# Kernel tuning notes

Measured on AMD Instinct MI355X. Metric: run time of the kernel, lower is better.

The kernel has to match this reference:

```python
import jax, jax.numpy as jnp
import numpy as np

N = 10000      # nodes
E = 65536      # edges
IN = 16        # in_channels
H = 64         # hidden_channels
ED = 4         # edge_attr_dim
MLP_H = 64     # hidden width of edge-weight MLPs


def _glorot(key, shape):
    fan_in, fan_out = shape[0], shape[1]
    lim = np.sqrt(6.0 / (fan_in + fan_out)).astype(np.float32)
    return jax.random.uniform(key, shape, jnp.float32, -lim, lim)


def setup_inputs() -> dict:
    key = jax.random.key(0)
    ks = jax.random.split(key, 16)
    x = jax.random.normal(ks[0], (N, IN), dtype=jnp.float32)
    edge_index = jax.random.randint(ks[1], (2, E), 0, N, dtype=jnp.int64)
    edge_attr = jax.random.normal(ks[2], (E, ED), dtype=jnp.float32)
    return {
        "x": x,
        "edge_index": edge_index,
        "edge_attr": edge_attr,
        # nn1: Linear(ED,64) -> ReLU -> Linear(64, IN*H)
        "nn1_w1": _glorot(ks[3], (ED, MLP_H)), "nn1_b1": jnp.zeros((MLP_H,), jnp.float32),
        "nn1_w2": _glorot(ks[4], (MLP_H, IN * H)), "nn1_b2": jnp.zeros((IN * H,), jnp.float32),
        "root1": _glorot(ks[5], (IN, H)), "bias1": jnp.zeros((H,), jnp.float32),
        # nn2: Linear(ED,64) -> ReLU -> Linear(64, H*H)
        "nn2_w1": _glorot(ks[6], (ED, MLP_H)), "nn2_b1": jnp.zeros((MLP_H,), jnp.float32),
        "nn2_w2": _glorot(ks[7], (MLP_H, H * H)), "nn2_b2": jnp.zeros((H * H,), jnp.float32),
        "root2": _glorot(ks[8], (H, H)), "bias2": jnp.zeros((H,), jnp.float32),
        # readout MLP
        "lin1_w": _glorot(ks[9], (H, 8)), "lin1_b": jnp.zeros((8,), jnp.float32),
        "lin2_w": _glorot(ks[10], (8, 1)), "lin2_b": jnp.zeros((1,), jnp.float32),
    }


def _nnconv(x, src, dst, edge_attr, w1, b1, w2, b2, root, bias, cin, cout):
    # Edge-conditioned weight generation: MLP(edge_attr) -> [E, cin, cout]
    h = jax.nn.relu(edge_attr @ w1 + b1)
    We = (h @ w2 + b2).reshape(-1, cin, cout)
    # Per-edge matmul: message_e = x[src_e] @ We_e  -> [E, cout]
    msg = jnp.einsum('ei,eio->eo', x[src], We)
    # Scatter mean over destination nodes
    s = jax.ops.segment_sum(msg, dst, num_segments=N)
    cnt = jax.ops.segment_sum(jnp.ones((msg.shape[0],), x.dtype), dst, num_segments=N)
    agg = s / jnp.maximum(cnt, 1.0)[:, None]
    # Root transform + bias (PyG NNConv defaults: root_weight=True, bias=True)
    return agg + x @ root + bias


def reference(x, edge_index, edge_attr,
              nn1_w1, nn1_b1, nn1_w2, nn1_b2, root1, bias1,
              nn2_w1, nn2_b1, nn2_w2, nn2_b2, root2, bias2,
              lin1_w, lin1_b, lin2_w, lin2_b):
    # Dropout layers are identity in eval mode.
    src, dst = edge_index[0], edge_index[1]
    h = jax.nn.relu(_nnconv(x, src, dst, edge_attr,
                            nn1_w1, nn1_b1, nn1_w2, nn1_b2, root1, bias1, IN, H))
    h = jax.nn.relu(_nnconv(h, src, dst, edge_attr,
                            nn2_w1, nn2_b1, nn2_w2, nn2_b2, root2, bias2, H, H))
    h = jax.nn.relu(h @ lin1_w + lin1_b)
    return (h @ lin2_w + lin2_b)[:, 0]  # squeeze(-1) -> [N]
```

## Files before the change

kernel.cpp:

```cpp
#include <hip/hip_runtime.h>
#include <hip/hip_bf16.h>

#define NN 10000
#define EE 65536

using short8  = __attribute__((ext_vector_type(8))) short;
using u16x8   = __attribute__((ext_vector_type(8))) unsigned short;
using float4v = __attribute__((ext_vector_type(4))) float;

__device__ __forceinline__ unsigned short f2b(float f){
  union { float f; unsigned int u; } v; v.f = f;
  unsigned int u = v.u;
  unsigned int r = (u + 0x7fff + ((u >> 16) & 1)) >> 16;
  return (unsigned short)r;
}



__device__ __forceinline__ void do_permB(int idx, const float* __restrict__ w2,
                                         unsigned short* __restrict__ Bt,
                                         int cin, int s , int cb ){
  int tile   = idx >> 9;
  int within = idx & 511;
  int ot  = tile >> s;
  int k32 = tile & ((1<<s)-1);
  int kklo = within & 7;
  int q    = within >> 3;
  int kkhi = q & 3;
  int orow = q >> 2;
  int o = ot*16 + orow;
  int k = k32*32 + kkhi*8 + kklo;
  int m = k >> cb;
  int i = k & (cin-1);
  Bt[idx] = f2b(w2[(size_t)m*(cin*64) + i*64 + o]);
}

__global__ __launch_bounds__(256) void k_prep(
    const float* __restrict__ w2a, unsigned short* __restrict__ Bt1,
    const float* __restrict__ w2b, unsigned short* __restrict__ Bt2,
    int* __restrict__ cnt){
  int b = blockIdx.x;
  int t = threadIdx.x;
  if(b < 40){
    int i = b*256 + t;
    if(i < NN) cnt[i] = 0;
  } else if(b < 296){
    do_permB((b-40)*256 + t, w2a, Bt1, 16, 5, 4);
  } else {
    do_permB((b-296)*256 + t, w2b, Bt2, 64, 7, 6);
  }
}


__global__ void k_hist(const int* __restrict__ dst, int* __restrict__ cnt){
  int e = blockIdx.x*256 + threadIdx.x;
  if(e < EE) atomicAdd(&cnt[dst[e]], 1);
}

__global__ __launch_bounds__(1024) void k_scan(const int* __restrict__ cnt, int* __restrict__ offs, int* __restrict__ cursor){
  const int T = 1024, PER = (NN + T - 1)/T;
  int tid = threadIdx.x;
  int base = tid*PER;
  int local[PER];
  int s = 0;
  #pragma unroll
  for(int j=0;j<PER;j++){
    int i = base+j;
    int v = (i<NN)? cnt[i] : 0;
    local[j] = s;
    s += v;
  }
  int lane = tid & 63, wv = tid >> 6;
  int val = s;
  #pragma unroll
  for(int o=1;o<64;o<<=1){
    int u = __shfl_up(val, o, 64);
    if(lane >= o) val += u;
  }
  __shared__ int wsum[16];
  if(lane==63) wsum[wv] = val;
  __syncthreads();
  if(tid==0){
    int acc=0;
    #pragma unroll
    for(int i=0;i<16;i++){ int t2=wsum[i]; wsum[i]=acc; acc+=t2; }
  }
  __syncthreads();
  int thr_excl = wsum[wv] + (val - s);
  #pragma unroll
  for(int j=0;j<PER;j++){
    int i = base+j;
    if(i<NN){ int e = thr_excl + local[j]; offs[i]=e; cursor[i]=e; }
  }
  if(tid == T-1) offs[NN] = thr_excl + s;
}

__global__ void k_scatter(const int* __restrict__ dst, const int* __restrict__ src,
                          int* __restrict__ cursor, int2* __restrict__ elist2){
  int e = blockIdx.x*256 + threadIdx.x;
  if(e < EE){ int p = atomicAdd(&cursor[dst[e]], 1); elist2[p] = make_int2(e, src[e]); }
}


__global__ __launch_bounds__(64) void k_accK1(const float* __restrict__ x,
    const int* __restrict__ offs, const int2* __restrict__ elist2,
    const float* __restrict__ ea, const float* __restrict__ w1, const float* __restrict__ b1,
    unsigned short* __restrict__ K1, float* __restrict__ XS, int v0){
  int v = v0 + blockIdx.x;
  int L = threadIdx.x;
  int cg = L & 3, mg = L >> 2;
  int i0 = cg << 2;
  float w1c0 = w1[L], w1c1 = w1[64+L], w1c2 = w1[128+L], w1c3 = w1[192+L];
  float b1c = b1[L];
  __shared__ float sh[2][64];
  float acc[4][4];
  #pragma unroll
  for(int j=0;j<4;j++)
    #pragma unroll
    for(int c=0;c<4;c++) acc[j][c]=0.f;
  float4 xs = make_float4(0.f,0.f,0.f,0.f);
  int p0 = offs[v], p1 = offs[v+1];
  float4 a_nxt = make_float4(0.f,0.f,0.f,0.f);
  float4 x_nxt = make_float4(0.f,0.f,0.f,0.f);
  if(p0 < p1){
    int2 es = elist2[p0];
    a_nxt = *(const float4*)(ea + (size_t)es.x*4);
    x_nxt = *(const float4*)(x + (size_t)es.y*16 + i0);
  }
  for(int p=p0;p<p1;p++){
    int buf = (p-p0)&1;
    float4 xv = x_nxt;
    float4 av = a_nxt;
    float hv = fmaxf(b1c + av.x*w1c0 + av.y*w1c1 + av.z*w1c2 + av.w*w1c3, 0.f);
    sh[buf][L] = hv;
    __syncthreads();
    if(p+1<p1){
      int2 es = elist2[p+1];
      a_nxt = *(const float4*)(ea + (size_t)es.x*4);
      x_nxt = *(const float4*)(x + (size_t)es.y*16 + i0);
    }
    xs.x += xv.x; xs.y += xv.y; xs.z += xv.z; xs.w += xv.w;
    #pragma unroll
    for(int j=0;j<4;j++){
      float hm = sh[buf][mg + 16*j];
      acc[j][0] += hm*xv.x; acc[j][1] += hm*xv.y;
      acc[j][2] += hm*xv.z; acc[j][3] += hm*xv.w;
    }
  }
  int r = blockIdx.x;
  int rt = r >> 4, lrow = r & 15;
  #pragma unroll
  for(int j=0;j<4;j++){
    int m = mg + 16*j;
    size_t sidx = ((size_t)(rt*32 + (m>>1)))*512
                + (size_t)lrow*32 + ((m&1)*2 + (cg>>1))*8 + ((cg&1)*4);
    ushort4 u;
    u.x=f2b(acc[j][0]); u.y=f2b(acc[j][1]); u.z=f2b(acc[j][2]); u.w=f2b(acc[j][3]);
    *(ushort4*)(K1 + sidx) = u;
  }
  if(mg==0) *(float4*)(XS + (size_t)v*64 + i0) = xs;
}


__global__ __launch_bounds__(64) void k_accK2(const float* __restrict__ x1,
    const int* __restrict__ offs, const int2* __restrict__ elist2,
    const float* __restrict__ ea, const float* __restrict__ w1, const float* __restrict__ b1,
    unsigned short* __restrict__ K, float* __restrict__ XS, int v0){
  int v = v0 + blockIdx.x;
  int L = threadIdx.x;
  int cg = L & 7, mg = L >> 3;
  int i0 = cg << 3;
  float w1c0 = w1[L], w1c1 = w1[64+L], w1c2 = w1[128+L], w1c3 = w1[192+L];
  float b1c = b1[L];
  __shared__ float sh[2][64];
  float acc[8][8];
  #pragma unroll
  for(int j=0;j<8;j++)
    #pragma unroll
    for(int c=0;c<8;c++) acc[j][c]=0.f;
  float4 xs0 = make_float4(0.f,0.f,0.f,0.f);
  float4 xs1 = make_float4(0.f,0.f,0.f,0.f);
  int p0 = offs[v], p1 = offs[v+1];
  float4 a_nxt = make_float4(0.f,0.f,0.f,0.f);
  float4 x_nxt0 = make_float4(0.f,0.f,0.f,0.f);
  float4 x_nxt1 = make_float4(0.f,0.f,0.f,0.f);
  if(p0 < p1){
    int2 es = elist2[p0];
    a_nxt = *(const float4*)(ea + (size_t)es.x*4);
    const float* xr = x1 + (size_t)es.y*64 + i0;
    x_nxt0 = *(const float4*)xr;
    x_nxt1 = *(const float4*)(xr+4);
  }
  for(int p=p0;p<p1;p++){
    int buf = (p-p0)&1;
    float4 xv0 = x_nxt0, xv1 = x_nxt1;
    float4 av = a_nxt;
    float hv = fmaxf(b1c + av.x*w1c0 + av.y*w1c1 + av.z*w1c2 + av.w*w1c3, 0.f);
    sh[buf][L] = hv;
    __syncthreads();
    if(p+1<p1){
      int2 es = elist2[p+1];
      a_nxt = *(const float4*)(ea + (size_t)es.x*4);
      const float* xr = x1 + (size_t)es.y*64 + i0;
      x_nxt0 = *(const float4*)xr;
      x_nxt1 = *(const float4*)(xr+4);
    }
    xs0.x += xv0.x; xs0.y += xv0.y; xs0.z += xv0.z; xs0.w += xv0.w;
    xs1.x += xv1.x; xs1.y += xv1.y; xs1.z += xv1.z; xs1.w += xv1.w;
    float4 h4a = *(float4*)&sh[buf][mg*8];
    float4 h4b = *(float4*)&sh[buf][mg*8+4];
    #pragma unroll
    for(int jj=0;jj<2;jj++){
      float4 h4 = jj? h4b : h4a;
      #pragma unroll
      for(int tq=0;tq<4;tq++){
        int j = jj*4+tq;
        float hm = (tq==0)?h4.x:(tq==1)?h4.y:(tq==2)?h4.z:h4.w;
        acc[j][0] += hm*xv0.x; acc[j][1] += hm*xv0.y;
        acc[j][2] += hm*xv0.z; acc[j][3] += hm*xv0.w;
        acc[j][4] += hm*xv1.x; acc[j][5] += hm*xv1.y;
        acc[j][6] += hm*xv1.z; acc[j][7] += hm*xv1.w;
      }
    }
  }
  int r = blockIdx.x;
  int rt = r >> 4, lrow = r & 15;
  #pragma unroll
  for(int j=0;j<8;j++){
    int m = mg*8 + j;
    size_t sidx = ((size_t)(rt*128 + m*2 + (cg>>2)))*512
                + (size_t)lrow*32 + (cg&3)*8;
    u16x8 u;
    #pragma unroll
    for(int c=0;c<8;c++) u[c] = f2b(acc[j][c]);
    *(u16x8*)(K + sidx) = u;
  }
  if(mg==0){
    *(float4*)(XS + (size_t)v*64 + i0)     = xs0;
    *(float4*)(XS + (size_t)v*64 + i0 + 4) = xs1;
  }
}


template<int T>
__global__ __launch_bounds__(256) void k_gemm_nl(const unsigned short* __restrict__ A,
    const unsigned short* __restrict__ Bt, float* __restrict__ P,
    int rows, int KT32){
  int tid = threadIdx.x;
  int lane = tid & 63;
  int w = tid >> 6;
  int rg = blockIdx.x;
  int b32 = (blockIdx.y*4 + w)*T;
  int lperm = (lane & 15)*32 + (lane >> 4)*8;
  const unsigned short* Ap = A  + (((size_t)rg*KT32 + b32) << 9) + lperm;
  const unsigned short* Bp = Bt + ((size_t)b32 << 9) + lperm;
  size_t bstep = (size_t)KT32 << 9;

  float4v acc0{}, acc1{}, acc2{}, acc3{};

  short8 a_all[T];
  #pragma unroll
  for(int t=0;t<T;t++) a_all[t] = *(const short8*)(Ap + t*512);

  short8 b0_c = *(const short8*)(Bp);
  short8 b1_c = *(const short8*)(Bp + bstep);
  short8 b2_c = *(const short8*)(Bp + bstep*2);
  short8 b3_c = *(const short8*)(Bp + bstep*3);

  #pragma unroll
  for(int t=0;t<T;t++){
    short8 b0_n=b0_c, b1_n=b1_c, b2_n=b2_c, b3_n=b3_c;
    if(t+1 < T){
      b0_n = *(const short8*)(Bp + (t+1)*512);
      b1_n = *(const short8*)(Bp + bstep   + (t+1)*512);
      b2_n = *(const short8*)(Bp + bstep*2 + (t+1)*512);
      b3_n = *(const short8*)(Bp + bstep*3 + (t+1)*512);
    }
    acc0 = __builtin_amdgcn_mfma_f32_16x16x32_bf16(a_all[t], b0_c, acc0, 0,0,0);
    acc1 = __builtin_amdgcn_mfma_f32_16x16x32_bf16(a_all[t], b1_c, acc1, 0,0,0);
    acc2 = __builtin_amdgcn_mfma_f32_16x16x32_bf16(a_all[t], b2_c, acc2, 0,0,0);
    acc3 = __builtin_amdgcn_mfma_f32_16x16x32_bf16(a_all[t], b3_c, acc3, 0,0,0);
    b0_c = b0_n; b1_c = b1_n; b2_c = b2_n; b3_c = b3_n;
  }

  __shared__ float4v sh4[4][4][64];
  sh4[w][0][lane] = acc0;
  sh4[w][1][lane] = acc1;
  sh4[w][2][lane] = acc2;
  sh4[w][3][lane] = acc3;
  __syncthreads();
  float4v r{};
  #pragma unroll
  for(int w2=0; w2<4; w2++){
    float4v v = sh4[w2][w][lane];
    r[0]+=v[0]; r[1]+=v[1]; r[2]+=v[2]; r[3]+=v[3];
  }
  int lrow = lane & 15;
  int quad = lane >> 4;
  float* Pr = P + (size_t)blockIdx.y*rows*64 + (size_t)(rg*16 + quad*4)*64 + w*16 + lrow;
  #pragma unroll
  for(int reg=0; reg<4; reg++) Pr[(size_t)reg*64] = r[reg];
}


template<int CIN, int SPLIT>
__global__ __launch_bounds__(256) void k_reduce_ep(const float* __restrict__ P, int rows, int v0,
    const float* __restrict__ XS, const float* __restrict__ b2, const float* __restrict__ xprev,
    const float* __restrict__ root, const float* __restrict__ bias, const int* __restrict__ offs,
    float* __restrict__ out){
  int idx = blockIdx.x*256 + threadIdx.x;
  if(idx >= rows*16) return;
  int r = idx >> 4, og = (idx & 15) << 2;
  int v = v0 + r;

  float4 s = make_float4(0.f,0.f,0.f,0.f);
  #pragma unroll
  for(int z=0; z<SPLIT; z++){
    float4 p = *(const float4*)(P + ((size_t)z*rows + r)*64 + og);
    s.x += p.x; s.y += p.y; s.z += p.z; s.w += p.w;
  }
  #pragma unroll
  for(int i=0;i<CIN;i++){
    float xsv = XS[(size_t)v*64 + i];
    float4 b = *(const float4*)(b2 + i*64 + og);
    s.x += xsv*b.x; s.y += xsv*b.y; s.z += xsv*b.z; s.w += xsv*b.w;
  }
  float4 rt = make_float4(0.f,0.f,0.f,0.f);
  #pragma unroll
  for(int i=0;i<CIN;i++){
    float xv = xprev[(size_t)v*CIN + i];
    float4 wv = *(const float4*)(root + i*64 + og);
    rt.x += xv*wv.x; rt.y += xv*wv.y; rt.z += xv*wv.z; rt.w += xv*wv.w;
  }
  float c = (float)(offs[v+1]-offs[v]); c = fmaxf(c, 1.f);
  float inv = 1.f/c;
  float4 bi = *(const float4*)(bias + og);
  float4 o;
  o.x = fmaxf(s.x*inv + rt.x + bi.x, 0.f);
  o.y = fmaxf(s.y*inv + rt.y + bi.y, 0.f);
  o.z = fmaxf(s.z*inv + rt.z + bi.z, 0.f);
  o.w = fmaxf(s.w*inv + rt.w + bi.w, 0.f);
  *(float4*)(out + (size_t)v*64 + og) = o;
}


template<int SPLIT>
__global__ __launch_bounds__(256) void k_red2_ro(const float* __restrict__ P, int rows,
    const float* __restrict__ XS, const float* __restrict__ b2, const float* __restrict__ x1,
    const float* __restrict__ root, const float* __restrict__ bias, const int* __restrict__ offs,
    const float* __restrict__ lw1, const float* __restrict__ lb1,
    const float* __restrict__ lw2, const float* __restrict__ lb2,
    float* __restrict__ out){
  __shared__ float row[16][68];
  __shared__ float hjs[16][8];
  int tid = threadIdx.x;
  int idx = blockIdx.x*256 + tid;
  int r = idx >> 4, og = (idx & 15) << 2;
  int n = tid >> 4;
  int nbase = blockIdx.x*16;
  int ninblk = rows - nbase; if(ninblk > 16) ninblk = 16;

  float4 o = make_float4(0.f,0.f,0.f,0.f);
  if(r < rows){
    float4 s = make_float4(0.f,0.f,0.f,0.f);
    #pragma unroll
    for(int z=0; z<SPLIT; z++){
      float4 p = *(const float4*)(P + ((size_t)z*rows + r)*64 + og);
      s.x += p.x; s.y += p.y; s.z += p.z; s.w += p.w;
    }
    #pragma unroll
    for(int i=0;i<64;i++){
      float xsv = XS[(size_t)r*64 + i];
      float4 b = *(const float4*)(b2 + i*64 + og);
      s.x += xsv*b.x; s.y += xsv*b.y; s.z += xsv*b.z; s.w += xsv*b.w;
    }
    float4 rt = make_float4(0.f,0.f,0.f,0.f);
    #pragma unroll
    for(int i=0;i<64;i++){
      float xv = x1[(size_t)r*64 + i];
      float4 wv = *(const float4*)(root + i*64 + og);
      rt.x += xv*wv.x; rt.y += xv*wv.y; rt.z += xv*wv.z; rt.w += xv*wv.w;
    }
    float c = (float)(offs[r+1]-offs[r]); c = fmaxf(c, 1.f);
    float inv = 1.f/c;
    float4 bi = *(const float4*)(bias + og);
    o.x = fmaxf(s.x*inv + rt.x + bi.x, 0.f);
    o.y = fmaxf(s.y*inv + rt.y + bi.y, 0.f);
    o.z = fmaxf(s.z*inv + rt.z + bi.z, 0.f);
    o.w = fmaxf(s.w*inv + rt.w + bi.w, 0.f);
  }
  *(float4*)&row[n][og] = o;
  __syncthreads();
  if(tid < 128){
    int n2 = tid >> 3, j = tid & 7;
    if(n2 < ninblk){
      float a = lb1[j];
      #pragma unroll
      for(int i=0;i<64;i++) a += row[n2][i]*lw1[i*8+j];
      hjs[n2][j] = fmaxf(a, 0.f)*lw2[j];
    }
  }
  __syncthreads();
  if(tid < 16 && tid < ninblk){
    float s = lb2[0];
    #pragma unroll
    for(int j=0;j<8;j++) s += hjs[tid][j];
    out[nbase + tid] = s;
  }
}


__global__ void k_readout(const float* __restrict__ x2, const float* __restrict__ lw1,
                          const float* __restrict__ lb1, const float* __restrict__ lw2,
                          const float* __restrict__ lb2, float* __restrict__ out){
  int v = blockIdx.x*256 + threadIdx.x;
  if(v >= NN) return;
  float accj[8];
  #pragma unroll
  for(int j=0;j<8;j++) accj[j] = lb1[j];
  const float* xr = x2 + (size_t)v*64;
  #pragma unroll 16
  for(int i=0;i<64;i++){
    float xv = xr[i];
    #pragma unroll
    for(int j=0;j<8;j++) accj[j] += xv*lw1[i*8+j];
  }
  float o = lb2[0];
  #pragma unroll
  for(int j=0;j<8;j++) o += fmaxf(accj[j],0.f)*lw2[j];
  out[v] = o;
}


extern "C" void kernel_launch(void* const* d_in, const int* in_sizes, int n_in,
                              void* d_out, int out_size, void* d_ws, size_t ws_size,
                              hipStream_t stream) {
  const float* x      = (const float*)d_in[0];
  const int*   ei     = (const int*)d_in[1];
  const float* ea     = (const float*)d_in[2];
  const float* nn1_w1 = (const float*)d_in[3];
  const float* nn1_b1 = (const float*)d_in[4];
  const float* nn1_w2 = (const float*)d_in[5];
  const float* nn1_b2 = (const float*)d_in[6];
  const float* root1  = (const float*)d_in[7];
  const float* bias1  = (const float*)d_in[8];
  const float* nn2_w1 = (const float*)d_in[9];
  const float* nn2_b1 = (const float*)d_in[10];
  const float* nn2_w2 = (const float*)d_in[11];
  const float* nn2_b2 = (const float*)d_in[12];
  const float* root2  = (const float*)d_in[13];
  const float* bias2  = (const float*)d_in[14];
  const float* lin1_w = (const float*)d_in[15];
  const float* lin1_b = (const float*)d_in[16];
  const float* lin2_w = (const float*)d_in[17];
  const float* lin2_b = (const float*)d_in[18];
  float* out = (float*)d_out;

  const int* srcIdx = ei;
  const int* dstIdx = ei + EE;

  char* w = (char*)d_ws;
  size_t off = 0;
  auto alloc = [&](size_t bytes)->void*{
    void* p = w + off;
    off = (off + bytes + 255) & ~(size_t)255;
    return p;
  };
  int*            cnt    = (int*)           alloc((size_t)NN*4);
  int*            offs   = (int*)           alloc((size_t)(NN+1)*4);
  int*            cursor = (int*)           alloc((size_t)NN*4);
  int2*           elist2 = (int2*)          alloc((size_t)EE*8);
  float*          XS     = (float*)         alloc((size_t)NN*64*4);
  float*          x1     = (float*)         alloc((size_t)NN*64*4);
  unsigned short* Bt1    = (unsigned short*)alloc((size_t)64*1024*2);
  unsigned short* Bt2    = (unsigned short*)alloc((size_t)64*4096*2);
  size_t fixedBytes = off;
  size_t R = (ws_size > fixedBytes) ? (ws_size - fixedBytes) : 0;

  const int S1 = 4, S2 = 4;
  size_t needSingle = (size_t)NN*4096*2 + (size_t)S2*NN*64*4;
  bool single = (R >= needSingle + 4096);

  k_prep   <<<1320, 256, 0, stream>>>(nn1_w2, Bt1, nn2_w2, Bt2, cnt);
  k_hist   <<<(EE+255)/256, 256, 0, stream>>>(dstIdx, cnt);
  k_scan   <<<1, 1024, 0, stream>>>(cnt, offs, cursor);
  k_scatter<<<(EE+255)/256, 256, 0, stream>>>(dstIdx, srcIdx, cursor, elist2);

  if(single){
    unsigned short* Kbuf = (unsigned short*)(w + off);
    float* P = (float*)(w + off + (size_t)NN*4096*2);

    k_accK1<<<NN, 64, 0, stream>>>(x, offs, elist2, ea, nn1_w1, nn1_b1, Kbuf, XS, 0);
    {
      dim3 g(NN/16, S1);
      k_gemm_nl<2><<<g, 256, 0, stream>>>(Kbuf, Bt1, P, NN, 32);
    }
    k_reduce_ep<16,S1><<<(NN*16+255)/256, 256, 0, stream>>>(P, NN, 0, XS, nn1_b2, x,
                                                             root1, bias1, offs, x1);
    k_accK2<<<NN, 64, 0, stream>>>(x1, offs, elist2, ea, nn2_w1, nn2_b1, Kbuf, XS, 0);
    {
      dim3 g(NN/16, S2);
      k_gemm_nl<8><<<g, 256, 0, stream>>>(Kbuf, Bt2, P, NN, 128);
    }
    k_red2_ro<S2><<<(NN+15)/16, 256, 0, stream>>>(P, NN, XS, nn2_b2, x1, root2, bias2, offs,
                                                   lin1_w, lin1_b, lin2_w, lin2_b, out);
  } else {
    float* x2b = (float*)alloc((size_t)NN*64*4);
    R = (ws_size > off) ? (ws_size - off) : 0;
    long long C2 = (long long)(R / (4096*2 + S2*64*4));
    long long C1 = (long long)(R / (1024*2 + S1*64*4));
    if(C2 > NN) C2 = NN; if(C1 > NN) C1 = NN;
    C2 &= ~63LL; C1 &= ~63LL;
    if(C2 < 128) C2 = 128; if(C1 < 128) C1 = 128;
    unsigned short* Kbuf = (unsigned short*)(w + off);
    {
      float* P = (float*)(w + off + (size_t)C1*1024*2);
      for(long long v0=0; v0<NN; v0+=C1){
        int rows = (int)((NN - v0 < C1) ? (NN - v0) : C1);
        k_accK1<<<rows, 64, 0, stream>>>(x, offs, elist2, ea, nn1_w1, nn1_b1, Kbuf, XS, (int)v0);
        dim3 g(rows/16, S1);
        k_gemm_nl<2><<<g, 256, 0, stream>>>(Kbuf, Bt1, P, rows, 32);
        k_reduce_ep<16,S1><<<(rows*16+255)/256, 256, 0, stream>>>(P, rows, (int)v0, XS, nn1_b2, x,
                                                                   root1, bias1, offs, x1);
      }
    }
    {
      float* P = (float*)(w + off + (size_t)C2*4096*2);
      for(long long v0=0; v0<NN; v0+=C2){
        int rows = (int)((NN - v0 < C2) ? (NN - v0) : C2);
        k_accK2<<<rows, 64, 0, stream>>>(x1, offs, elist2, ea, nn2_w1, nn2_b1, Kbuf, XS, (int)v0);
        dim3 g(rows/16, S2);
        k_gemm_nl<8><<<g, 256, 0, stream>>>(Kbuf, Bt2, P, rows, 128);
        k_reduce_ep<64,S2><<<(rows*16+255)/256, 256, 0, stream>>>(P, rows, (int)v0, XS, nn2_b2, x1,
                                                                   root2, bias2, offs, x2b);
      }
    }
    k_readout<<<(NN+255)/256, 256, 0, stream>>>(x2b, lin1_w, lin1_b, lin2_w, lin2_b, out);
  }
}
```

Measured before the change: 207.6 us.

## Fuse reduction epilogue into GEMM, drop split-K partial buffer

Removes the split-K grid dimension so each 16-row block computes the full K reduction across its four waves. The bias, root-transform, mean and ReLU epilogue (and the readout MLP for layer 2) are folded directly into the GEMM kernels. This eliminates the partial-sum buffer P, its global writes and reads, and two kernel launches per layer. The trade-off is fewer blocks (625 instead of 2500), each doing a longer serial MFMA chain, and the B/K tile permutation layout also changes.

```diff
diff --git a/kernel.cpp b/kernel.cpp
--- a/kernel.cpp
+++ b/kernel.cpp
@@ -24,12 +24,10 @@
   int within = idx & 511;
   int ot  = tile >> s;
   int k32 = tile & ((1<<s)-1);
-  int kklo = within & 7;
-  int q    = within >> 3;
-  int kkhi = q & 3;
-  int orow = q >> 2;
+  int kk   = within & 31;
+  int orow = within >> 5;
   int o = ot*16 + orow;
-  int k = k32*32 + kkhi*8 + kklo;
+  int k = k32*32 + kk;
   int m = k >> cb;
   int i = k & (cin-1);
   Bt[idx] = f2b(w2[(size_t)m*(cin*64) + i*64 + o]);
@@ -153,7 +151,7 @@
   for(int j=0;j<4;j++){
     int m = mg + 16*j;
     size_t sidx = ((size_t)(rt*32 + (m>>1)))*512
-                + (size_t)lrow*32 + ((m&1)*2 + (cg>>1))*8 + ((cg&1)*4);
+                + (size_t)lrow*32 + (m&1)*16 + cg*4;
     ushort4 u;
     u.x=f2b(acc[j][0]); u.y=f2b(acc[j][1]); u.z=f2b(acc[j][2]); u.w=f2b(acc[j][3]);
     *(ushort4*)(K1 + sidx) = u;
@@ -242,45 +240,45 @@
 }
 
 
-template<int T>
-__global__ __launch_bounds__(256) void k_gemm_nl(const unsigned short* __restrict__ A,
-    const unsigned short* __restrict__ Bt, float* __restrict__ P,
-    int rows, int KT32){
+__global__ __launch_bounds__(256) void k_gemmF1(const unsigned short* __restrict__ A,
+    const unsigned short* __restrict__ Bt,
+    const float* __restrict__ XS, const float* __restrict__ eb,
+    const float* __restrict__ xp, const float* __restrict__ rw,
+    const float* __restrict__ bw, const int* __restrict__ offs,
+    float* __restrict__ x1out, int v0){
   int tid = threadIdx.x;
   int lane = tid & 63;
   int w = tid >> 6;
   int rg = blockIdx.x;
-  int b32 = (blockIdx.y*4 + w)*T;
   int lperm = (lane & 15)*32 + (lane >> 4)*8;
-  const unsigned short* Ap = A  + (((size_t)rg*KT32 + b32) << 9) + lperm;
-  const unsigned short* Bp = Bt + ((size_t)b32 << 9) + lperm;
-  size_t bstep = (size_t)KT32 << 9;
+  const unsigned short* Ap = A  + (((size_t)rg*32 + w*8) << 9) + lperm;
+  const unsigned short* Bp = Bt + (((size_t)w*8) << 9) + lperm;
+  size_t bstep = (size_t)32 << 9;
 
   float4v acc0{}, acc1{}, acc2{}, acc3{};
-
-  short8 a_all[T];
-  #pragma unroll
-  for(int t=0;t<T;t++) a_all[t] = *(const short8*)(Ap + t*512);
-
-  short8 b0_c = *(const short8*)(Bp);
-  short8 b1_c = *(const short8*)(Bp + bstep);
-  short8 b2_c = *(const short8*)(Bp + bstep*2);
-  short8 b3_c = *(const short8*)(Bp + bstep*3);
-
-  #pragma unroll
-  for(int t=0;t<T;t++){
-    short8 b0_n=b0_c, b1_n=b1_c, b2_n=b2_c, b3_n=b3_c;
-    if(t+1 < T){
-      b0_n = *(const short8*)(Bp + (t+1)*512);
-      b1_n = *(const short8*)(Bp + bstep   + (t+1)*512);
-      b2_n = *(const short8*)(Bp + bstep*2 + (t+1)*512);
-      b3_n = *(const short8*)(Bp + bstep*3 + (t+1)*512);
-    }
-    acc0 = __builtin_amdgcn_mfma_f32_16x16x32_bf16(a_all[t], b0_c, acc0, 0,0,0);
-    acc1 = __builtin_amdgcn_mfma_f32_16x16x32_bf16(a_all[t], b1_c, acc1, 0,0,0);
-    acc2 = __builtin_amdgcn_mfma_f32_16x16x32_bf16(a_all[t], b2_c, acc2, 0,0,0);
-    acc3 = __builtin_amdgcn_mfma_f32_16x16x32_bf16(a_all[t], b3_c, acc3, 0,0,0);
-    b0_c = b0_n; b1_c = b1_n; b2_c = b2_n; b3_c = b3_n;
+  short8 a_all[8];
+  #pragma unroll
+  for(int t=0;t<8;t++) a_all[t] = *(const short8*)(Ap + t*512);
+
+  short8 b0c = *(const short8*)(Bp);
+  short8 b1c = *(const short8*)(Bp + bstep);
+  short8 b2c = *(const short8*)(Bp + bstep*2);
+  short8 b3c = *(const short8*)(Bp + bstep*3);
+
+  #pragma unroll
+  for(int t=0;t<8;t++){
+    short8 b0n=b0c, b1n=b1c, b2n=b2c, b3n=b3c;
+    if(t+1 < 8){
+      b0n = *(const short8*)(Bp + (t+1)*512);
+      b1n = *(const short8*)(Bp + bstep   + (t+1)*512);
+      b2n = *(const short8*)(Bp + bstep*2 + (t+1)*512);
+      b3n = *(const short8*)(Bp + bstep*3 + (t+1)*512);
+    }
+    acc0 = __builtin_amdgcn_mfma_f32_16x16x32_bf16(a_all[t], b0c, acc0, 0,0,0);
+    acc1 = __builtin_amdgcn_mfma_f32_16x16x32_bf16(a_all[t], b1c, acc1, 0,0,0);
+    acc2 = __builtin_amdgcn_mfma_f32_16x16x32_bf16(a_all[t], b2c, acc2, 0,0,0);
+    acc3 = __builtin_amdgcn_mfma_f32_16x16x32_bf16(a_all[t], b3c, acc3, 0,0,0);
+    b0c=b0n; b1c=b1n; b2c=b2n; b3c=b3n;
   }
 
   __shared__ float4v sh4[4][4][64];
@@ -292,143 +290,142 @@
   float4v r{};
   #pragma unroll
   for(int w2=0; w2<4; w2++){
-    float4v v = sh4[w2][w][lane];
-    r[0]+=v[0]; r[1]+=v[1]; r[2]+=v[2]; r[3]+=v[3];
-  }
-  int lrow = lane & 15;
-  int quad = lane >> 4;
-  float* Pr = P + (size_t)blockIdx.y*rows*64 + (size_t)(rg*16 + quad*4)*64 + w*16 + lrow;
-  #pragma unroll
-  for(int reg=0; reg<4; reg++) Pr[(size_t)reg*64] = r[reg];
-}
-
-
-template<int CIN, int SPLIT>
-__global__ __launch_bounds__(256) void k_reduce_ep(const float* __restrict__ P, int rows, int v0,
-    const float* __restrict__ XS, const float* __restrict__ b2, const float* __restrict__ xprev,
-    const float* __restrict__ root, const float* __restrict__ bias, const int* __restrict__ offs,
-    float* __restrict__ out){
-  int idx = blockIdx.x*256 + threadIdx.x;
-  if(idx >= rows*16) return;
-  int r = idx >> 4, og = (idx & 15) << 2;
-  int v = v0 + r;
-
-  float4 s = make_float4(0.f,0.f,0.f,0.f);
-  #pragma unroll
-  for(int z=0; z<SPLIT; z++){
-    float4 p = *(const float4*)(P + ((size_t)z*rows + r)*64 + og);
-    s.x += p.x; s.y += p.y; s.z += p.z; s.w += p.w;
-  }
-  #pragma unroll
-  for(int i=0;i<CIN;i++){
-    float xsv = XS[(size_t)v*64 + i];
-    float4 b = *(const float4*)(b2 + i*64 + og);
-    s.x += xsv*b.x; s.y += xsv*b.y; s.z += xsv*b.z; s.w += xsv*b.w;
-  }
-  float4 rt = make_float4(0.f,0.f,0.f,0.f);
-  #pragma unroll
-  for(int i=0;i<CIN;i++){
-    float xv = xprev[(size_t)v*CIN + i];
-    float4 wv = *(const float4*)(root + i*64 + og);
-    rt.x += xv*wv.x; rt.y += xv*wv.y; rt.z += xv*wv.z; rt.w += xv*wv.w;
-  }
-  float c = (float)(offs[v+1]-offs[v]); c = fmaxf(c, 1.f);
-  float inv = 1.f/c;
-  float4 bi = *(const float4*)(bias + og);
-  float4 o;
-  o.x = fmaxf(s.x*inv + rt.x + bi.x, 0.f);
-  o.y = fmaxf(s.y*inv + rt.y + bi.y, 0.f);
-  o.z = fmaxf(s.z*inv + rt.z + bi.z, 0.f);
-  o.w = fmaxf(s.w*inv + rt.w + bi.w, 0.f);
-  *(float4*)(out + (size_t)v*64 + og) = o;
-}
-
-
-template<int SPLIT>
-__global__ __launch_bounds__(256) void k_red2_ro(const float* __restrict__ P, int rows,
-    const float* __restrict__ XS, const float* __restrict__ b2, const float* __restrict__ x1,
-    const float* __restrict__ root, const float* __restrict__ bias, const int* __restrict__ offs,
+    float4v t = sh4[w2][w][lane];
+    r[0]+=t[0]; r[1]+=t[1]; r[2]+=t[2]; r[3]+=t[3];
+  }
+
+  int lrow = lane & 15, quad = lane >> 4;
+  int c = w*16 + lrow;
+  int vb = v0 + rg*16 + quad*4;
+  float s0=r[0], s1=r[1], s2=r[2], s3=r[3];
+  float t0=0.f, t1=0.f, t2=0.f, t3=0.f;
+  #pragma unroll
+  for(int i=0;i<16;i++){
+    float bv = eb[i*64 + c];
+    float rv = rw[i*64 + c];
+    s0 += XS[(size_t)vb*64       + i]*bv;  t0 += xp[(size_t)vb*16       + i]*rv;
+    s1 += XS[(size_t)(vb+1)*64   + i]*bv;  t1 += xp[(size_t)(vb+1)*16   + i]*rv;
+    s2 += XS[(size_t)(vb+2)*64   + i]*bv;  t2 += xp[(size_t)(vb+2)*16   + i]*rv;
+    s3 += XS[(size_t)(vb+3)*64   + i]*bv;  t3 += xp[(size_t)(vb+3)*16   + i]*rv;
+  }
+  float bc = bw[c];
+  #pragma unroll
+  for(int reg=0; reg<4; reg++){
+    int v = vb + reg;
+    float s = (reg==0)?s0:(reg==1)?s1:(reg==2)?s2:s3;
+    float t = (reg==0)?t0:(reg==1)?t1:(reg==2)?t2:t3;
+    float dg = fmaxf((float)(offs[v+1]-offs[v]), 1.f);
+    x1out[(size_t)v*64 + c] = fmaxf(s/dg + t + bc, 0.f);
+  }
+}
+
+
+__global__ __launch_bounds__(256) void k_gemmF2(const unsigned short* __restrict__ A,
+    const unsigned short* __restrict__ Bt,
+    const float* __restrict__ XS, const float* __restrict__ eb,
+    const float* __restrict__ x1p, const float* __restrict__ rw,
+    const float* __restrict__ bw, const int* __restrict__ offs,
     const float* __restrict__ lw1, const float* __restrict__ lb1,
     const float* __restrict__ lw2, const float* __restrict__ lb2,
-    float* __restrict__ out){
-  __shared__ float row[16][68];
+    float* __restrict__ out, int v0){
+  int tid = threadIdx.x;
+  int lane = tid & 63;
+  int w = tid >> 6;
+  int rg = blockIdx.x;
+  int lperm = (lane & 15)*32 + (lane >> 4)*8;
+  const unsigned short* Ap = A  + (((size_t)rg*128 + w*32) << 9) + lperm;
+  const unsigned short* Bp = Bt + (((size_t)w*32) << 9) + lperm;
+  size_t bstep = (size_t)128 << 9;
+
+  float4v acc0{}, acc1{}, acc2{}, acc3{};
+  short8 aA = *(const short8*)(Ap);
+  short8 aB = *(const short8*)(Ap + 512);
+  short8 aC = *(const short8*)(Ap + 1024);
+  short8 aD = *(const short8*)(Ap + 1536);
+  short8 b0c = *(const short8*)(Bp);
+  short8 b1c = *(const short8*)(Bp + bstep);
+  short8 b2c = *(const short8*)(Bp + bstep*2);
+  short8 b3c = *(const short8*)(Bp + bstep*3);
+
+#define GSTEP(AREG, TT) { \
+    short8 b0n=b0c, b1n=b1c, b2n=b2c, b3n=b3c; \
+    if((TT)+1 < 32){ \
+      b0n = *(const short8*)(Bp + ((TT)+1)*512); \
+      b1n = *(const short8*)(Bp + bstep   + ((TT)+1)*512); \
+      b2n = *(const short8*)(Bp + bstep*2 + ((TT)+1)*512); \
+      b3n = *(const short8*)(Bp + bstep*3 + ((TT)+1)*512); \
+    } \
+    acc0 = __builtin_amdgcn_mfma_f32_16x16x32_bf16(AREG, b0c, acc0, 0,0,0); \
+    acc1 = __builtin_amdgcn_mfma_f32_16x16x32_bf16(AREG, b1c, acc1, 0,0,0); \
+    acc2 = __builtin_amdgcn_mfma_f32_16x16x32_bf16(AREG, b2c, acc2, 0,0,0); \
+    acc3 = __builtin_amdgcn_mfma_f32_16x16x32_bf16(AREG, b3c, acc3, 0,0,0); \
+    if((TT)+4 < 32) AREG = *(const short8*)(Ap + ((TT)+4)*512); \
+    b0c=b0n; b1c=b1n; b2c=b2n; b3c=b3n; }
+
+  #pragma unroll
+  for(int g=0; g<8; g++){
+    GSTEP(aA, g*4+0)
+    GSTEP(aB, g*4+1)
+    GSTEP(aC, g*4+2)
+    GSTEP(aD, g*4+3)
+  }
+#undef GSTEP
+
+  __shared__ float4v sh4[4][4][64];
+  sh4[w][0][lane] = acc0;
+  sh4[w][1][lane] = acc1;
+  sh4[w][2][lane] = acc2;
+  sh4[w][3][lane] = acc3;
+  __syncthreads();
+  float4v r{};
+  #pragma unroll
+  for(int w2=0; w2<4; w2++){
+    float4v t = sh4[w2][w][lane];
+    r[0]+=t[0]; r[1]+=t[1]; r[2]+=t[2]; r[3]+=t[3];
+  }
+
+  __shared__ float rowsh[16][68];
   __shared__ float hjs[16][8];
-  int tid = threadIdx.x;
-  int idx = blockIdx.x*256 + tid;
-  int r = idx >> 4, og = (idx & 15) << 2;
-  int n = tid >> 4;
-  int nbase = blockIdx.x*16;
-  int ninblk = rows - nbase; if(ninblk > 16) ninblk = 16;
-
-  float4 o = make_float4(0.f,0.f,0.f,0.f);
-  if(r < rows){
-    float4 s = make_float4(0.f,0.f,0.f,0.f);
-    #pragma unroll
-    for(int z=0; z<SPLIT; z++){
-      float4 p = *(const float4*)(P + ((size_t)z*rows + r)*64 + og);
-      s.x += p.x; s.y += p.y; s.z += p.z; s.w += p.w;
-    }
-    #pragma unroll
-    for(int i=0;i<64;i++){
-      float xsv = XS[(size_t)r*64 + i];
-      float4 b = *(const float4*)(b2 + i*64 + og);
-      s.x += xsv*b.x; s.y += xsv*b.y; s.z += xsv*b.z; s.w += xsv*b.w;
-    }
-    float4 rt = make_float4(0.f,0.f,0.f,0.f);
-    #pragma unroll
-    for(int i=0;i<64;i++){
-      float xv = x1[(size_t)r*64 + i];
-      float4 wv = *(const float4*)(root + i*64 + og);
-      rt.x += xv*wv.x; rt.y += xv*wv.y; rt.z += xv*wv.z; rt.w += xv*wv.w;
-    }
-    float c = (float)(offs[r+1]-offs[r]); c = fmaxf(c, 1.f);
-    float inv = 1.f/c;
-    float4 bi = *(const float4*)(bias + og);
-    o.x = fmaxf(s.x*inv + rt.x + bi.x, 0.f);
-    o.y = fmaxf(s.y*inv + rt.y + bi.y, 0.f);
-    o.z = fmaxf(s.z*inv + rt.z + bi.z, 0.f);
-    o.w = fmaxf(s.w*inv + rt.w + bi.w, 0.f);
-  }
-  *(float4*)&row[n][og] = o;
+
+  int lrow = lane & 15, quad = lane >> 4;
+  int c = w*16 + lrow;
+  int rl0 = quad*4;
+  int vb = v0 + rg*16 + rl0;
+  float s0=r[0], s1=r[1], s2=r[2], s3=r[3];
+  float t0=0.f, t1=0.f, t2=0.f, t3=0.f;
+  #pragma unroll 8
+  for(int i=0;i<64;i++){
+    float bv = eb[i*64 + c];
+    float rv = rw[i*64 + c];
+    s0 += XS[(size_t)vb*64     + i]*bv;  t0 += x1p[(size_t)vb*64     + i]*rv;
+    s1 += XS[(size_t)(vb+1)*64 + i]*bv;  t1 += x1p[(size_t)(vb+1)*64 + i]*rv;
+    s2 += XS[(size_t)(vb+2)*64 + i]*bv;  t2 += x1p[(size_t)(vb+2)*64 + i]*rv;
+    s3 += XS[(size_t)(vb+3)*64 + i]*bv;  t3 += x1p[(size_t)(vb+3)*64 + i]*rv;
+  }
+  float bc = bw[c];
+  #pragma unroll
+  for(int reg=0; reg<4; reg++){
+    int v = vb + reg;
+    float s = (reg==0)?s0:(reg==1)?s1:(reg==2)?s2:s3;
+    float t = (reg==0)?t0:(reg==1)?t1:(reg==2)?t2:t3;
+    float dg = fmaxf((float)(offs[v+1]-offs[v]), 1.f);
+    rowsh[rl0+reg][c] = fmaxf(s/dg + t + bc, 0.f);
+  }
   __syncthreads();
   if(tid < 128){
     int n2 = tid >> 3, j = tid & 7;
-    if(n2 < ninblk){
-      float a = lb1[j];
-      #pragma unroll
-      for(int i=0;i<64;i++) a += row[n2][i]*lw1[i*8+j];
-      hjs[n2][j] = fmaxf(a, 0.f)*lw2[j];
-    }
+    float a = lb1[j];
+    #pragma unroll
+    for(int i=0;i<64;i++) a += rowsh[n2][i]*lw1[i*8+j];
+    hjs[n2][j] = fmaxf(a, 0.f)*lw2[j];
   }
   __syncthreads();
-  if(tid < 16 && tid < ninblk){
+  if(tid < 16){
     float s = lb2[0];
     #pragma unroll
     for(int j=0;j<8;j++) s += hjs[tid][j];
-    out[nbase + tid] = s;
-  }
-}
-
-
-__global__ void k_readout(const float* __restrict__ x2, const float* __restrict__ lw1,
-                          const float* __restrict__ lb1, const float* __restrict__ lw2,
-                          const float* __restrict__ lb2, float* __restrict__ out){
-  int v = blockIdx.x*256 + threadIdx.x;
-  if(v >= NN) return;
-  float accj[8];
-  #pragma unroll
-  for(int j=0;j<8;j++) accj[j] = lb1[j];
-  const float* xr = x2 + (size_t)v*64;
-  #pragma unroll 16
-  for(int i=0;i<64;i++){
-    float xv = xr[i];
-    #pragma unroll
-    for(int j=0;j<8;j++) accj[j] += xv*lw1[i*8+j];
-  }
-  float o = lb2[0];
-  #pragma unroll
-  for(int j=0;j<8;j++) o += fmaxf(accj[j],0.f)*lw2[j];
-  out[v] = o;
+    out[v0 + rg*16 + tid] = s;
+  }
 }
 
 
@@ -477,8 +474,7 @@
   size_t fixedBytes = off;
   size_t R = (ws_size > fixedBytes) ? (ws_size - fixedBytes) : 0;
 
-  const int S1 = 4, S2 = 4;
-  size_t needSingle = (size_t)NN*4096*2 + (size_t)S2*NN*64*4;
+  size_t needSingle = (size_t)(NN/16)*128*1024;
   bool single = (R >= needSingle + 4096);
 
   k_prep   <<<1320, 256, 0, stream>>>(nn1_w2, Bt1, nn2_w2, Bt2, cnt);
@@ -488,53 +484,29 @@
 
   if(single){
     unsigned short* Kbuf = (unsigned short*)(w + off);
-    float* P = (float*)(w + off + (size_t)NN*4096*2);
-
-    k_accK1<<<NN, 64, 0, stream>>>(x, offs, elist2, ea, nn1_w1, nn1_b1, Kbuf, XS, 0);
-    {
-      dim3 g(NN/16, S1);
-      k_gemm_nl<2><<<g, 256, 0, stream>>>(Kbuf, Bt1, P, NN, 32);
-    }
-    k_reduce_ep<16,S1><<<(NN*16+255)/256, 256, 0, stream>>>(P, NN, 0, XS, nn1_b2, x,
-                                                             root1, bias1, offs, x1);
-    k_accK2<<<NN, 64, 0, stream>>>(x1, offs, elist2, ea, nn2_w1, nn2_b1, Kbuf, XS, 0);
-    {
-      dim3 g(NN/16, S2);
-      k_gemm_nl<8><<<g, 256, 0, stream>>>(Kbuf, Bt2, P, NN, 128);
-    }
-    k_red2_ro<S2><<<(NN+15)/16, 256, 0, stream>>>(P, NN, XS, nn2_b2, x1, root2, bias2, offs,
-                                                   lin1_w, lin1_b, lin2_w, lin2_b, out);
+
+    k_accK1 <<<NN, 64, 0, stream>>>(x, offs, elist2, ea, nn1_w1, nn1_b1, Kbuf, XS, 0);
+    k_gemmF1<<<NN/16, 256, 0, stream>>>(Kbuf, Bt1, XS, nn1_b2, x, root1, bias1, offs, x1, 0);
+    k_accK2 <<<NN, 64, 0, stream>>>(x1, offs, elist2, ea, nn2_w1, nn2_b1, Kbuf, XS, 0);
+    k_gemmF2<<<NN/16, 256, 0, stream>>>(Kbuf, Bt2, XS, nn2_b2, x1, root2, bias2, offs,
+                                        lin1_w, lin1_b, lin2_w, lin2_b, out, 0);
   } else {
-    float* x2b = (float*)alloc((size_t)NN*64*4);
-    R = (ws_size > off) ? (ws_size - off) : 0;
-    long long C2 = (long long)(R / (4096*2 + S2*64*4));
-    long long C1 = (long long)(R / (1024*2 + S1*64*4));
+    long long C2 = (long long)(R / 8192);
+    long long C1 = (long long)(R / 2048);
     if(C2 > NN) C2 = NN; if(C1 > NN) C1 = NN;
     C2 &= ~63LL; C1 &= ~63LL;
     if(C2 < 128) C2 = 128; if(C1 < 128) C1 = 128;
     unsigned short* Kbuf = (unsigned short*)(w + off);
-    {
-      float* P = (float*)(w + off + (size_t)C1*1024*2);
-      for(long long v0=0; v0<NN; v0+=C1){
-        int rows = (int)((NN - v0 < C1) ? (NN - v0) : C1);
-        k_accK1<<<rows, 64, 0, stream>>>(x, offs, elist2, ea, nn1_w1, nn1_b1, Kbuf, XS, (int)v0);
-        dim3 g(rows/16, S1);
-        k_gemm_nl<2><<<g, 256, 0, stream>>>(Kbuf, Bt1, P, rows, 32);
-        k_reduce_ep<16,S1><<<(rows*16+255)/256, 256, 0, stream>>>(P, rows, (int)v0, XS, nn1_b2, x,
-                                                                   root1, bias1, offs, x1);
-      }
-    }
-    {
-      float* P = (float*)(w + off + (size_t)C2*4096*2);
-      for(long long v0=0; v0<NN; v0+=C2){
-        int rows = (int)((NN - v0 < C2) ? (NN - v0) : C2);
-        k_accK2<<<rows, 64, 0, stream>>>(x1, offs, elist2, ea, nn2_w1, nn2_b1, Kbuf, XS, (int)v0);
-        dim3 g(rows/16, S2);
-        k_gemm_nl<8><<<g, 256, 0, stream>>>(Kbuf, Bt2, P, rows, 128);
-        k_reduce_ep<64,S2><<<(rows*16+255)/256, 256, 0, stream>>>(P, rows, (int)v0, XS, nn2_b2, x1,
-                                                                   root2, bias2, offs, x2b);
-      }
-    }
-    k_readout<<<(NN+255)/256, 256, 0, stream>>>(x2b, lin1_w, lin1_b, lin2_w, lin2_b, out);
-  }
-}
+    for(long long v0=0; v0<NN; v0+=C1){
+      int rows = (int)((NN - v0 < C1) ? (NN - v0) : C1);
+      k_accK1 <<<rows, 64, 0, stream>>>(x, offs, elist2, ea, nn1_w1, nn1_b1, Kbuf, XS, (int)v0);
+      k_gemmF1<<<rows/16, 256, 0, stream>>>(Kbuf, Bt1, XS, nn1_b2, x, root1, bias1, offs, x1, (int)v0);
+    }
+    for(long long v0=0; v0<NN; v0+=C2){
+      int rows = (int)((NN - v0 < C2) ? (NN - v0) : C2);
+      k_accK2 <<<rows, 64, 0, stream>>>(x1, offs, elist2, ea, nn2_w1, nn2_b1, Kbuf, XS, (int)v0);
+      k_gemmF2<<<rows/16, 256, 0, stream>>>(Kbuf, Bt2, XS, nn2_b2, x1, root2, bias2, offs,
+                                            lin1_w, lin1_b, lin2_w, lin2_b, out, (int)v0);
+    }
+  }
+}
```

New measurement: 213.7 us. 1.03x slower.

## Restructure MFMA GEMM to stage B tiles in LDS, drop cross-wave reduction

Applied to the files above, without the earlier changes.

The GEMM kernel is replaced by one where each 512-thread block loads its K-slice of the B matrix into shared memory once. Each of 8 waves then owns a separate 16-row tile and accumulates all four 16-column output tiles directly, so the shared-memory cross-wave reduction goes away. A tiles are streamed with nontemporal loads through a 4-deep register prefetch, and the layer-2 split-K factor rises to 8. The B permutation and K1 write layout are changed to a simpler contiguous k ordering, the chunked fallback path now fuses the readout into the reduce, and the larger split adds partial-sum traffic.

```diff
diff --git a/kernel.cpp b/kernel.cpp
--- a/kernel.cpp
+++ b/kernel.cpp
@@ -13,6 +13,10 @@
   unsigned int u = v.u;
   unsigned int r = (u + 0x7fff + ((u >> 16) & 1)) >> 16;
   return (unsigned short)r;
+}
+
+__device__ __forceinline__ short8 ntload(const unsigned short* p){
+  return __builtin_nontemporal_load((const short8*)p);
 }
 
 
@@ -24,12 +28,10 @@
   int within = idx & 511;
   int ot  = tile >> s;
   int k32 = tile & ((1<<s)-1);
-  int kklo = within & 7;
-  int q    = within >> 3;
-  int kkhi = q & 3;
-  int orow = q >> 2;
+  int kk   = within & 31;
+  int orow = within >> 5;
   int o = ot*16 + orow;
-  int k = k32*32 + kkhi*8 + kklo;
+  int k = k32*32 + kk;
   int m = k >> cb;
   int i = k & (cin-1);
   Bt[idx] = f2b(w2[(size_t)m*(cin*64) + i*64 + o]);
@@ -153,7 +155,7 @@
   for(int j=0;j<4;j++){
     int m = mg + 16*j;
     size_t sidx = ((size_t)(rt*32 + (m>>1)))*512
-                + (size_t)lrow*32 + ((m&1)*2 + (cg>>1))*8 + ((cg&1)*4);
+                + (size_t)lrow*32 + (m&1)*16 + cg*4;
     ushort4 u;
     u.x=f2b(acc[j][0]); u.y=f2b(acc[j][1]); u.z=f2b(acc[j][2]); u.w=f2b(acc[j][3]);
     *(ushort4*)(K1 + sidx) = u;
@@ -242,64 +244,63 @@
 }
 
 
-template<int T>
-__global__ __launch_bounds__(256) void k_gemm_nl(const unsigned short* __restrict__ A,
+template<int KT32, int TSTEPS>
+__global__ __launch_bounds__(512) void k_gemmS(const unsigned short* __restrict__ A,
     const unsigned short* __restrict__ Bt, float* __restrict__ P,
-    int rows, int KT32){
+    int ntiles, int rowsChunk){
+  __shared__ unsigned short Bs[4*TSTEPS*512];
   int tid = threadIdx.x;
   int lane = tid & 63;
   int w = tid >> 6;
-  int rg = blockIdx.x;
-  int b32 = (blockIdx.y*4 + w)*T;
+  int s = blockIdx.y;
+  int kbase = s*TSTEPS;
+
+  constexpr int NT = 4*TSTEPS;
+  constexpr int PERW = NT/8;
+  #pragma unroll
+  for(int it=0; it<PERW; it++){
+    int g = w*PERW + it;
+    int ct = g / TSTEPS, t = g - ct*TSTEPS;
+    *(short8*)(Bs + (size_t)g*512 + lane*8) =
+        *(const short8*)(Bt + (((size_t)ct*KT32 + kbase + t) << 9) + lane*8);
+  }
+  __syncthreads();
+
+  int lrt = blockIdx.x*8 + w;
+  if(lrt >= ntiles) return;
+
   int lperm = (lane & 15)*32 + (lane >> 4)*8;
-  const unsigned short* Ap = A  + (((size_t)rg*KT32 + b32) << 9) + lperm;
-  const unsigned short* Bp = Bt + ((size_t)b32 << 9) + lperm;
-  size_t bstep = (size_t)KT32 << 9;
+  const unsigned short* Ap = A + (((size_t)lrt*KT32 + kbase) << 9) + lperm;
+  const unsigned short* BsL = Bs + lperm;
 
   float4v acc0{}, acc1{}, acc2{}, acc3{};
-
-  short8 a_all[T];
-  #pragma unroll
-  for(int t=0;t<T;t++) a_all[t] = *(const short8*)(Ap + t*512);
-
-  short8 b0_c = *(const short8*)(Bp);
-  short8 b1_c = *(const short8*)(Bp + bstep);
-  short8 b2_c = *(const short8*)(Bp + bstep*2);
-  short8 b3_c = *(const short8*)(Bp + bstep*3);
-
-  #pragma unroll
-  for(int t=0;t<T;t++){
-    short8 b0_n=b0_c, b1_n=b1_c, b2_n=b2_c, b3_n=b3_c;
-    if(t+1 < T){
-      b0_n = *(const short8*)(Bp + (t+1)*512);
-      b1_n = *(const short8*)(Bp + bstep   + (t+1)*512);
-      b2_n = *(const short8*)(Bp + bstep*2 + (t+1)*512);
-      b3_n = *(const short8*)(Bp + bstep*3 + (t+1)*512);
-    }
-    acc0 = __builtin_amdgcn_mfma_f32_16x16x32_bf16(a_all[t], b0_c, acc0, 0,0,0);
-    acc1 = __builtin_amdgcn_mfma_f32_16x16x32_bf16(a_all[t], b1_c, acc1, 0,0,0);
-    acc2 = __builtin_amdgcn_mfma_f32_16x16x32_bf16(a_all[t], b2_c, acc2, 0,0,0);
-    acc3 = __builtin_amdgcn_mfma_f32_16x16x32_bf16(a_all[t], b3_c, acc3, 0,0,0);
-    b0_c = b0_n; b1_c = b1_n; b2_c = b2_n; b3_c = b3_n;
-  }
-
-  __shared__ float4v sh4[4][4][64];
-  sh4[w][0][lane] = acc0;
-  sh4[w][1][lane] = acc1;
-  sh4[w][2][lane] = acc2;
-  sh4[w][3][lane] = acc3;
-  __syncthreads();
-  float4v r{};
-  #pragma unroll
-  for(int w2=0; w2<4; w2++){
-    float4v v = sh4[w2][w][lane];
-    r[0]+=v[0]; r[1]+=v[1]; r[2]+=v[2]; r[3]+=v[3];
-  }
-  int lrow = lane & 15;
-  int quad = lane >> 4;
-  float* Pr = P + (size_t)blockIdx.y*rows*64 + (size_t)(rg*16 + quad*4)*64 + w*16 + lrow;
-  #pragma unroll
-  for(int reg=0; reg<4; reg++) Pr[(size_t)reg*64] = r[reg];
+  short8 ab[4];
+  #pragma unroll
+  for(int t=0;t<4;t++) ab[t] = ntload(Ap + t*512);
+
+  #pragma unroll
+  for(int t=0;t<TSTEPS;t++){
+    short8 a  = ab[t&3];
+    short8 b0 = *(const short8*)(BsL + (0*TSTEPS+t)*512);
+    short8 b1 = *(const short8*)(BsL + (1*TSTEPS+t)*512);
+    short8 b2 = *(const short8*)(BsL + (2*TSTEPS+t)*512);
+    short8 b3 = *(const short8*)(BsL + (3*TSTEPS+t)*512);
+    acc0 = __builtin_amdgcn_mfma_f32_16x16x32_bf16(a, b0, acc0, 0,0,0);
+    acc1 = __builtin_amdgcn_mfma_f32_16x16x32_bf16(a, b1, acc1, 0,0,0);
+    acc2 = __builtin_amdgcn_mfma_f32_16x16x32_bf16(a, b2, acc2, 0,0,0);
+    acc3 = __builtin_amdgcn_mfma_f32_16x16x32_bf16(a, b3, acc3, 0,0,0);
+    if(t+4 < TSTEPS) ab[t&3] = ntload(Ap + (t+4)*512);
+  }
+
+  int lrow = lane & 15, quad = lane >> 4;
+  float* Pr = P + ((size_t)s*rowsChunk + lrt*16 + quad*4)*64 + lrow;
+  #pragma unroll
+  for(int reg=0;reg<4;reg++){
+    Pr[(size_t)reg*64 +  0] = acc0[reg];
+    Pr[(size_t)reg*64 + 16] = acc1[reg];
+    Pr[(size_t)reg*64 + 32] = acc2[reg];
+    Pr[(size_t)reg*64 + 48] = acc3[reg];
+  }
 }
 
 
@@ -345,7 +346,7 @@
 
 
 template<int SPLIT>
-__global__ __launch_bounds__(256) void k_red2_ro(const float* __restrict__ P, int rows,
+__global__ __launch_bounds__(256) void k_red2_ro(const float* __restrict__ P, int rows, int v0,
     const float* __restrict__ XS, const float* __restrict__ b2, const float* __restrict__ x1,
     const float* __restrict__ root, const float* __restrict__ bias, const int* __restrict__ offs,
     const float* __restrict__ lw1, const float* __restrict__ lb1,
@@ -362,6 +363,7 @@
 
   float4 o = make_float4(0.f,0.f,0.f,0.f);
   if(r < rows){
+    int vg = v0 + r;
     float4 s = make_float4(0.f,0.f,0.f,0.f);
     #pragma unroll
     for(int z=0; z<SPLIT; z++){
@@ -370,18 +372,18 @@
     }
     #pragma unroll
     for(int i=0;i<64;i++){
-      float xsv = XS[(size_t)r*64 + i];
+      float xsv = XS[(size_t)vg*64 + i];
       float4 b = *(const float4*)(b2 + i*64 + og);
       s.x += xsv*b.x; s.y += xsv*b.y; s.z += xsv*b.z; s.w += xsv*b.w;
     }
     float4 rt = make_float4(0.f,0.f,0.f,0.f);
     #pragma unroll
     for(int i=0;i<64;i++){
-      float xv = x1[(size_t)r*64 + i];
+      float xv = x1[(size_t)vg*64 + i];
       float4 wv = *(const float4*)(root + i*64 + og);
       rt.x += xv*wv.x; rt.y += xv*wv.y; rt.z += xv*wv.z; rt.w += xv*wv.w;
     }
-    float c = (float)(offs[r+1]-offs[r]); c = fmaxf(c, 1.f);
+    float c = (float)(offs[vg+1]-offs[vg]); c = fmaxf(c, 1.f);
     float inv = 1.f/c;
     float4 bi = *(const float4*)(bias + og);
     o.x = fmaxf(s.x*inv + rt.x + bi.x, 0.f);
@@ -405,30 +407,8 @@
     float s = lb2[0];
     #pragma unroll
     for(int j=0;j<8;j++) s += hjs[tid][j];
-    out[nbase + tid] = s;
-  }
-}
-
-
-__global__ void k_readout(const float* __restrict__ x2, const float* __restrict__ lw1,
-                          const float* __restrict__ lb1, const float* __restrict__ lw2,
-                          const float* __restrict__ lb2, float* __restrict__ out){
-  int v = blockIdx.x*256 + threadIdx.x;
-  if(v >= NN) return;
-  float accj[8];
-  #pragma unroll
-  for(int j=0;j<8;j++) accj[j] = lb1[j];
-  const float* xr = x2 + (size_t)v*64;
-  #pragma unroll 16
-  for(int i=0;i<64;i++){
-    float xv = xr[i];
-    #pragma unroll
-    for(int j=0;j<8;j++) accj[j] += xv*lw1[i*8+j];
-  }
-  float o = lb2[0];
-  #pragma unroll
-  for(int j=0;j<8;j++) o += fmaxf(accj[j],0.f)*lw2[j];
-  out[v] = o;
+    out[v0 + nbase + tid] = s;
+  }
 }
 
 
@@ -477,8 +457,8 @@
   size_t fixedBytes = off;
   size_t R = (ws_size > fixedBytes) ? (ws_size - fixedBytes) : 0;
 
-  const int S1 = 4, S2 = 4;
-  size_t needSingle = (size_t)NN*4096*2 + (size_t)S2*NN*64*4;
+  const int S1 = 4, S2 = 8;
+  size_t needSingle = (size_t)(NN/16)*128*1024 + (size_t)S2*NN*64*4;
   bool single = (R >= needSingle + 4096);
 
   k_prep   <<<1320, 256, 0, stream>>>(nn1_w2, Bt1, nn2_w2, Bt2, cnt);
@@ -488,53 +468,47 @@
 
   if(single){
     unsigned short* Kbuf = (unsigned short*)(w + off);
-    float* P = (float*)(w + off + (size_t)NN*4096*2);
-
-    k_accK1<<<NN, 64, 0, stream>>>(x, offs, elist2, ea, nn1_w1, nn1_b1, Kbuf, XS, 0);
-    {
-      dim3 g(NN/16, S1);
-      k_gemm_nl<2><<<g, 256, 0, stream>>>(Kbuf, Bt1, P, NN, 32);
-    }
+    float* P = (float*)(w + off + (size_t)(NN/16)*128*1024);
+    int ntiles = NN/16;
+    int gx = (ntiles + 7)/8;
+
+    k_accK1 <<<NN, 64, 0, stream>>>(x, offs, elist2, ea, nn1_w1, nn1_b1, Kbuf, XS, 0);
+    k_gemmS<32,8> <<<dim3(gx, S1), 512, 0, stream>>>(Kbuf, Bt1, P, ntiles, NN);
     k_reduce_ep<16,S1><<<(NN*16+255)/256, 256, 0, stream>>>(P, NN, 0, XS, nn1_b2, x,
                                                              root1, bias1, offs, x1);
-    k_accK2<<<NN, 64, 0, stream>>>(x1, offs, elist2, ea, nn2_w1, nn2_b1, Kbuf, XS, 0);
-    {
-      dim3 g(NN/16, S2);
-      k_gemm_nl<8><<<g, 256, 0, stream>>>(Kbuf, Bt2, P, NN, 128);
-    }
-    k_red2_ro<S2><<<(NN+15)/16, 256, 0, stream>>>(P, NN, XS, nn2_b2, x1, root2, bias2, offs,
+    k_accK2 <<<NN, 64, 0, stream>>>(x1, offs, elist2, ea, nn2_w1, nn2_b1, Kbuf, XS, 0);
+    k_gemmS<128,16><<<dim3(gx, S2), 512, 0, stream>>>(Kbuf, Bt2, P, ntiles, NN);
+    k_red2_ro<S2><<<(NN+15)/16, 256, 0, stream>>>(P, NN, 0, XS, nn2_b2, x1, root2, bias2, offs,
                                                    lin1_w, lin1_b, lin2_w, lin2_b, out);
   } else {
-    float* x2b = (float*)alloc((size_t)NN*64*4);
-    R = (ws_size > off) ? (ws_size - off) : 0;
-    long long C2 = (long long)(R / (4096*2 + S2*64*4));
-    long long C1 = (long long)(R / (1024*2 + S1*64*4));
+    long long C2 = (long long)(R / (8192 + S2*256));
+    long long C1 = (long long)(R / (2048 + S1*256));
     if(C2 > NN) C2 = NN; if(C1 > NN) C1 = NN;
-    C2 &= ~63LL; C1 &= ~63LL;
+    C2 &= ~127LL; C1 &= ~127LL;
     if(C2 < 128) C2 = 128; if(C1 < 128) C1 = 128;
     unsigned short* Kbuf = (unsigned short*)(w + off);
     {
-      float* P = (float*)(w + off + (size_t)C1*1024*2);
+      float* P = (float*)(w + off + (size_t)C1*2048);
       for(long long v0=0; v0<NN; v0+=C1){
         int rows = (int)((NN - v0 < C1) ? (NN - v0) : C1);
+        int nt = rows/16, gx = (nt + 7)/8;
         k_accK1<<<rows, 64, 0, stream>>>(x, offs, elist2, ea, nn1_w1, nn1_b1, Kbuf, XS, (int)v0);
-        dim3 g(rows/16, S1);
-        k_gemm_nl<2><<<g, 256, 0, stream>>>(Kbuf, Bt1, P, rows, 32);
+        k_gemmS<32,8><<<dim3(gx, S1), 512, 0, stream>>>(Kbuf, Bt1, P, nt, rows);
         k_reduce_ep<16,S1><<<(rows*16+255)/256, 256, 0, stream>>>(P, rows, (int)v0, XS, nn1_b2, x,
                                                                    root1, bias1, offs, x1);
       }
     }
     {
-      float* P = (float*)(w + off + (size_t)C2*4096*2);
+      float* P = (float*)(w + off + (size_t)C2*8192);
       for(long long v0=0; v0<NN; v0+=C2){
         int rows = (int)((NN - v0 < C2) ? (NN - v0) : C2);
+        int nt = rows/16, gx = (nt + 7)/8;
         k_accK2<<<rows, 64, 0, stream>>>(x1, offs, elist2, ea, nn2_w1, nn2_b1, Kbuf, XS, (int)v0);
-        dim3 g(rows/16, S2);
-        k_gemm_nl<8><<<g, 256, 0, stream>>>(Kbuf, Bt2, P, rows, 128);
-        k_reduce_ep<64,S2><<<(rows*16+255)/256, 256, 0, stream>>>(P, rows, (int)v0, XS, nn2_b2, x1,
-                                                                   root2, bias2, offs, x2b);
+        k_gemmS<128,16><<<dim3(gx, S2), 512, 0, stream>>>(Kbuf, Bt2, P, nt, rows);
+        k_red2_ro<S2><<<(rows+15)/16, 256, 0, stream>>>(P, rows, (int)v0, XS, nn2_b2, x1,
+                                                         root2, bias2, offs,
+                                                         lin1_w, lin1_b, lin2_w, lin2_b, out);
       }
     }
-    k_readout<<<(NN+255)/256, 256, 0, stream>>>(x2b, lin1_w, lin1_b, lin2_w, lin2_b, out);
-  }
-}
+  }
+}
```

Result: no change. 206.5 us (median of 2 runs) (-0.5%).
